# Optimization experiments

Hardware: AMD Instinct MI355X
Metric: run time of the kernel (lower is better)

Reference implementation:

```python
import jax, jax.numpy as jnp
import numpy as np

# config dims (see shape_source)
NO = 8        # Max_Object
NT = 32       # Max_Time
C = 512       # feat_dims
VD = 1024     # visual_dim
RD = 300      # self.nfeat (relation word-vector dim)
H = 4         # headnum
B = 8         # batch
No = NT * 2 * NO      # 512 object-graph nodes
Nr = NT * NO * NO     # 2048 relation-graph nodes


def _glorot(key, shape):
    fan_in = shape[0]
    return jax.random.normal(key, shape, dtype=jnp.float32) / np.sqrt(fan_in)


def setup_inputs() -> dict:
    key = jax.random.key(0)
    ks = jax.random.split(key, 18)
    inp = {
        "Ao": jax.random.uniform(ks[0], (B, No, No), dtype=jnp.float32),
        "srco": jax.random.normal(ks[1], (B, 1, 1, No, VD), dtype=jnp.float32),
        "Ar": jax.random.uniform(ks[2], (B, Nr, Nr), dtype=jnp.float32),
        "srcr": jax.random.normal(ks[3], (B, 1, 1, Nr, RD), dtype=jnp.float32),
        # GraphConvolution weights: gcl_o/gcl2_o and gcl_r/gcl2_r
        "Wo1": _glorot(ks[4], (VD, 1024)),
        "Wo2": _glorot(ks[5], (1024, C)),
        "Wr1": _glorot(ks[6], (RD, 1024)),
        "Wr2": _glorot(ks[7], (1024, C)),
        # MultiHeadAttention (e2n) projections
        "Wq": _glorot(ks[8], (C, C)), "bq": jnp.zeros((C,), jnp.float32),
        "Wk": _glorot(ks[9], (C, C)), "bk": jnp.zeros((C,), jnp.float32),
        "Wv": _glorot(ks[10], (C, C)), "bv": jnp.zeros((C,), jnp.float32),
        "Wp": _glorot(ks[11], (C, C)), "bp": jnp.zeros((C,), jnp.float32),
        # e2n_embed: Linear(2C -> C)
        "We": _glorot(ks[12], (2 * C, C)), "be": jnp.zeros((C,), jnp.float32),
    }
    return inp


def _gcn2(A, x, W1, W2):
    """Two stacked GraphConvolution layers with self-loops: relu((A+I) @ x @ W).
    A: (b,N,N), x: (b,N,Din). Vectorized over batch (torch code loops per-sample)."""
    eye = jnp.eye(A.shape[-1], dtype=A.dtype)
    Ah = A + eye
    h = jax.nn.relu(jnp.einsum('bij,bjd->bid', Ah, x @ W1))
    return jax.nn.relu(jnp.einsum('bij,bjd->bid', Ah, h @ W2))


def _mha(x, Wq, bq, Wk, bk, Wv, bv, Wp, bp):
    """Standard multi-head self-attention. x: (Bseg, S, C)."""
    Bs, S, _ = x.shape
    dh = C // H
    q = (x @ Wq + bq).reshape(Bs, S, H, dh)
    k = (x @ Wk + bk).reshape(Bs, S, H, dh)
    v = (x @ Wv + bv).reshape(Bs, S, H, dh)
    attn = jax.nn.softmax(jnp.einsum('bqhd,bkhd->bhqk', q, k) / np.sqrt(dh), axis=-1)
    o = jnp.einsum('bhqk,bkhd->bqhd', attn, v).reshape(Bs, S, C)
    return o @ Wp + bp


def _forward(Ao, srco, Ar, srcr, Wo1, Wo2, Wr1, Wr2,
             Wq, bq, Wk, bk, Wv, bv, Wp, bp, We, be):
    b = Ao.shape[0]
    # object-graph GCN (torch loops over batch; vectorized here)
    xo = srco[:, 0, 0, :, :VD]                       # (b, No, VD)
    srco_gcn = _gcn2(Ao, xo, Wo1, Wo2)               # (b, No, C)
    out_gcn_o = srco_gcn.reshape(b, NT, 2 * NO, C)
    # relation-graph GCN
    xr = srcr[:, 0, 0]                               # (b, Nr, RD)
    srcr_gcn = _gcn2(Ar, xr, Wr1, Wr2)               # (b, Nr, C)
    out_gcn_r = srcr_gcn.reshape(b, NT, NO * NO, C)
    # compute_e2n: segment-wise MHA over NO-token windows (torch loops over NO)
    r = out_gcn_r.reshape(b * NT, NO, NO, C)
    seg_a = r.reshape(b * NT * NO, NO, C)                      # rows of NOxNO grid
    a = _mha(seg_a, Wq, bq, Wk, bk, Wv, bv, Wp, bp).mean(axis=1)
    a = a.reshape(b * NT, NO, C)
    seg_o = jnp.swapaxes(r, 1, 2).reshape(b * NT * NO, NO, C)  # cols (permute 0,2,1,3)
    o = _mha(seg_o, Wq, bq, Wk, bk, Wv, bv, Wp, bp).mean(axis=1)
    o = o.reshape(b * NT, NO, C)
    tmp = jnp.concatenate([a, o], axis=1)                      # (b*NT, 2*NO, C)
    cat = jnp.concatenate([tmp, out_gcn_o.reshape(b * NT, 2 * NO, C)], axis=-1)
    out_e2n = cat @ We + be
    return out_e2n.reshape(b, NT, 2 * NO, C)


def reference(Ao, srco, Ar, srcr, Wo1, Wo2, Wr1, Wr2,
              Wq, bq, Wk, bk, Wv, bv, Wp, bp, We, be):
    return _forward(Ao, srco, Ar, srcr, Wo1, Wo2, Wr1, Wr2,
                    Wq, bq, Wk, bk, Wv, bv, Wp, bp, We, be)
```

## Files before the change

kernel.cpp:

```cpp
#include <hip/hip_runtime.h>
#include <hip/hip_bf16.h>


typedef __attribute__((ext_vector_type(4))) float f32x4;
typedef __attribute__((ext_vector_type(8))) short bf16x8s;

#define TILE 128
#define BKK 32
#define LDSS 40
#define LDSL 32

#if __has_builtin(__builtin_amdgcn_global_load_lds)
#define HAVE_GLL 1
#else
#define HAVE_GLL 0
#endif

__device__ inline void gll16(const __hip_bfloat16* g, __hip_bfloat16* l) {
#if HAVE_GLL
    __builtin_amdgcn_global_load_lds(
        (const __attribute__((address_space(1))) void*)g,
        (__attribute__((address_space(3))) void*)l,
        16, 0, 0);
#endif
}

__device__ inline void split2(float a, float b, unsigned& h, unsigned& l) {
    __hip_bfloat16 ha = __float2bfloat16(a), hb = __float2bfloat16(b);
    float ra = __bfloat162float(ha), rb = __bfloat162float(hb);
    __hip_bfloat16 la = __float2bfloat16(a - ra), lb = __float2bfloat16(b - rb);
    unsigned short uha = *(unsigned short*)&ha, uhb = *(unsigned short*)&hb;
    unsigned short ula = *(unsigned short*)&la, ulb = *(unsigned short*)&lb;
    h = (unsigned)uha | ((unsigned)uhb << 16);
    l = (unsigned)ula | ((unsigned)ulb << 16);
}

__device__ inline void splitw(float v, unsigned short& h, unsigned short& l) {
    __hip_bfloat16 hb = __float2bfloat16(v);
    __hip_bfloat16 lb = __float2bfloat16(v - __bfloat162float(hb));
    h = *(unsigned short*)&hb;
    l = *(unsigned short*)&lb;
}

__device__ inline void swz_block(int& bx, int& by, int& bz) {
    int gx = gridDim.x, gy = gridDim.y;
    int nwg = gx * gy * gridDim.z;
    int flat = bx + gx * (by + gy * bz);
    int cpx = nwg >> 3;
    int w = (flat & 7) * cpx + (flat >> 3);
    bx = w % gx;
    int t = w / gx;
    by = t % gy;
    bz = t / gy;
}

__global__ __launch_bounds__(256) void gemm_planes(
    const __hip_bfloat16* __restrict__ Aph, const __hip_bfloat16* __restrict__ Apl,
    long long sA, int lda,
    const __hip_bfloat16* __restrict__ BTh, const __hip_bfloat16* __restrict__ BTl,
    long long sBT, int ldbt,
    void* __restrict__ D, __hip_bfloat16* __restrict__ Dl_, long long sD, int ldd,
    const float* __restrict__ addN, long long sAddN, int ldaddN,
    const __hip_bfloat16* __restrict__ addTh, const __hip_bfloat16* __restrict__ addTl,
    long long sAddT, int ldaddT,
    const float* __restrict__ bias,
    int K, int relu, int outMode)
{
    __shared__ __hip_bfloat16 AhB[2][TILE * LDSL], AlB[2][TILE * LDSL];
    __shared__ __hip_bfloat16 BhB[2][TILE * LDSL], BlB[2][TILE * LDSL];

    int bx = blockIdx.x, by = blockIdx.y, bz = blockIdx.z;
    swz_block(bx, by, bz);

    const int tid  = threadIdx.x;
    const int lane = tid & 63;
    const int wave = tid >> 6;
    const int wm   = (wave >> 1) * 64;
    const int wn   = (wave & 1) * 64;
    const int row0 = by * TILE;
    const int col0 = bx * TILE;
    const int b    = bz;

    const __hip_bfloat16* Abh = Aph + (size_t)b * sA;
    const __hip_bfloat16* Abl = Apl + (size_t)b * sA;
    const __hip_bfloat16* Bbh = BTh + (size_t)b * sBT;
    const __hip_bfloat16* Bbl = BTl + (size_t)b * sBT;

    f32x4 acc[4][4];
#pragma unroll
    for (int i = 0; i < 4; ++i)
#pragma unroll
        for (int j = 0; j < 4; ++j) acc[i][j] = (f32x4){0.f, 0.f, 0.f, 0.f};

    const int quad = lane >> 4;
    const int l16  = lane & 15;

    const int m0  = wave * 16 + (lane >> 2);
    const int m1  = (wave + 4) * 16 + (lane >> 2);
    const int sl  = lane & 3;
    const int kq0 = sl ^ ((m0 >> 1) & 3);
    const int kq1 = sl ^ ((m1 >> 1) & 3);
    const size_t gA0 = (size_t)(row0 + m0) * lda + kq0 * 8;
    const size_t gA1 = (size_t)(row0 + m1) * lda + kq1 * 8;
    const size_t gB0 = (size_t)(col0 + m0) * ldbt + kq0 * 8;
    const size_t gB1 = (size_t)(col0 + m1) * ldbt + kq1 * 8;
    const int ldsc0 = wave * 512;
    const int ldsc1 = (wave + 4) * 512;

#if HAVE_GLL
#define STAGE(buf, kk) do { \
    gll16(Abh + gA0 + (kk), &AhB[buf][ldsc0]); \
    gll16(Abh + gA1 + (kk), &AhB[buf][ldsc1]); \
    gll16(Abl + gA0 + (kk), &AlB[buf][ldsc0]); \
    gll16(Abl + gA1 + (kk), &AlB[buf][ldsc1]); \
    gll16(Bbh + gB0 + (kk), &BhB[buf][ldsc0]); \
    gll16(Bbh + gB1 + (kk), &BhB[buf][ldsc1]); \
    gll16(Bbl + gB0 + (kk), &BlB[buf][ldsc0]); \
    gll16(Bbl + gB1 + (kk), &BlB[buf][ldsc1]); \
} while (0)
#define WAITVM8() asm volatile("s_waitcnt vmcnt(8)" ::: "memory")
#define WAITVM0() asm volatile("s_waitcnt vmcnt(0)" ::: "memory")
#else
#define STAGE(buf, kk) do { \
    *(uint4*)(&AhB[buf][m0 * LDSL + sl * 8]) = *(const uint4*)(Abh + gA0 + (kk)); \
    *(uint4*)(&AhB[buf][m1 * LDSL + sl * 8]) = *(const uint4*)(Abh + gA1 + (kk)); \
    *(uint4*)(&AlB[buf][m0 * LDSL + sl * 8]) = *(const uint4*)(Abl + gA0 + (kk)); \
    *(uint4*)(&AlB[buf][m1 * LDSL + sl * 8]) = *(const uint4*)(Abl + gA1 + (kk)); \
    *(uint4*)(&BhB[buf][m0 * LDSL + sl * 8]) = *(const uint4*)(Bbh + gB0 + (kk)); \
    *(uint4*)(&BhB[buf][m1 * LDSL + sl * 8]) = *(const uint4*)(Bbh + gB1 + (kk)); \
    *(uint4*)(&BlB[buf][m0 * LDSL + sl * 8]) = *(const uint4*)(Bbl + gB0 + (kk)); \
    *(uint4*)(&BlB[buf][m1 * LDSL + sl * 8]) = *(const uint4*)(Bbl + gB1 + (kk)); \
} while (0)
#define WAITVM8() asm volatile("" ::: "memory")
#define WAITVM0() asm volatile("" ::: "memory")
#endif

    const int nt = K / BKK;
    int cur = 0;

    STAGE(0, 0);
    STAGE(1, BKK);

    for (int t = 0; t < nt; ++t) {
        if (t + 1 < nt) { WAITVM8(); } else { WAITVM0(); }
        __builtin_amdgcn_s_barrier();

        const __hip_bfloat16* Ah = AhB[cur];
        const __hip_bfloat16* Al = AlB[cur];
        const __hip_bfloat16* Bh = BhB[cur];
        const __hip_bfloat16* Bl = BlB[cur];

        bf16x8s bhf[4], blf[4];
#pragma unroll
        for (int nt2 = 0; nt2 < 4; ++nt2) {
            int r = wn + nt2 * 16 + l16;
            int ss = (quad ^ ((r >> 1) & 3)) * 8;
            bhf[nt2] = *(const bf16x8s*)(&Bh[r * LDSL + ss]);
            blf[nt2] = *(const bf16x8s*)(&Bl[r * LDSL + ss]);
        }
#pragma unroll
        for (int mt = 0; mt < 4; ++mt) {
            int r = wm + mt * 16 + l16;
            int ss = (quad ^ ((r >> 1) & 3)) * 8;
            bf16x8s ahf = *(const bf16x8s*)(&Ah[r * LDSL + ss]);
            bf16x8s alf = *(const bf16x8s*)(&Al[r * LDSL + ss]);
#pragma unroll
            for (int nt2 = 0; nt2 < 4; ++nt2) {
                acc[mt][nt2] = __builtin_amdgcn_mfma_f32_16x16x32_bf16(ahf, bhf[nt2], acc[mt][nt2], 0, 0, 0);
                acc[mt][nt2] = __builtin_amdgcn_mfma_f32_16x16x32_bf16(ahf, blf[nt2], acc[mt][nt2], 0, 0, 0);
                acc[mt][nt2] = __builtin_amdgcn_mfma_f32_16x16x32_bf16(alf, bhf[nt2], acc[mt][nt2], 0, 0, 0);
            }
        }

        __builtin_amdgcn_s_barrier();
        if (t + 2 < nt) STAGE(cur, (t + 2) * BKK);
        cur ^= 1;
    }
#undef STAGE
#undef WAITVM8
#undef WAITVM0

    float* DbF = (float*)D + (size_t)b * sD;
    __hip_bfloat16* Dhb = (__hip_bfloat16*)D + (size_t)b * sD;
    __hip_bfloat16* Dlb = Dl_ ? Dl_ + (size_t)b * sD : nullptr;
    const float* AddN = addN ? addN + (size_t)b * sAddN : nullptr;
    const __hip_bfloat16* ATh = addTh ? addTh + (size_t)b * sAddT : nullptr;
    const __hip_bfloat16* ATl = addTl ? addTl + (size_t)b * sAddT : nullptr;
#pragma unroll
    for (int mt = 0; mt < 4; ++mt)
#pragma unroll
        for (int nt2 = 0; nt2 < 4; ++nt2)
#pragma unroll
            for (int r = 0; r < 4; ++r) {
                int m = row0 + wm + mt * 16 + quad * 4 + r;
                int n = col0 + wn + nt2 * 16 + l16;
                float v = acc[mt][nt2][r];
                if (AddN) v += AddN[(size_t)m * ldaddN + n];
                if (ATh) v += __bfloat162float(ATh[(size_t)n * ldaddT + m])
                            + __bfloat162float(ATl[(size_t)n * ldaddT + m]);
                if (bias) v += bias[n];
                if (relu && v < 0.f) v = 0.f;
                if (outMode == 0) {
                    DbF[(size_t)m * ldd + n] = v;
                } else {
                    unsigned short hh, ll;
                    splitw(v, hh, ll);
                    size_t o = (size_t)m * ldd + n;
                    *(unsigned short*)&Dhb[o] = hh;
                    *(unsigned short*)&Dlb[o] = ll;
                }
            }
}

__global__ __launch_bounds__(256) void gemm_bf16t(
    const __hip_bfloat16* __restrict__ A, int lda,
    const __hip_bfloat16* __restrict__ BT, int ldbt,
    void* __restrict__ D, int ldd,
    const float* __restrict__ bias,
    int K, int outF32)
{
    __shared__ __hip_bfloat16 AsB[2][TILE * LDSL];
    __shared__ __hip_bfloat16 BsB[2][TILE * LDSL];

    int bx = blockIdx.x, by = blockIdx.y, bz = blockIdx.z;
    swz_block(bx, by, bz);

    const int tid  = threadIdx.x;
    const int lane = tid & 63;
    const int wave = tid >> 6;
    const int wm   = (wave >> 1) * 64;
    const int wn   = (wave & 1) * 64;
    const int row0 = by * TILE;
    const int col0 = bx * TILE;

    f32x4 acc[4][4];
#pragma unroll
    for (int i = 0; i < 4; ++i)
#pragma unroll
        for (int j = 0; j < 4; ++j) acc[i][j] = (f32x4){0.f, 0.f, 0.f, 0.f};

    const int quad = lane >> 4;
    const int l16  = lane & 15;

    const int m0  = wave * 16 + (lane >> 2);
    const int m1  = (wave + 4) * 16 + (lane >> 2);
    const int sl  = lane & 3;
    const int kq0 = sl ^ ((m0 >> 1) & 3);
    const int kq1 = sl ^ ((m1 >> 1) & 3);
    const size_t gA0 = (size_t)(row0 + m0) * lda + kq0 * 8;
    const size_t gA1 = (size_t)(row0 + m1) * lda + kq1 * 8;
    const size_t gB0 = (size_t)(col0 + m0) * ldbt + kq0 * 8;
    const size_t gB1 = (size_t)(col0 + m1) * ldbt + kq1 * 8;
    const int ldsc0 = wave * 512;
    const int ldsc1 = (wave + 4) * 512;

#if HAVE_GLL
#define STAGE1(buf, kk) do { \
    gll16(A + gA0 + (kk), &AsB[buf][ldsc0]); \
    gll16(A + gA1 + (kk), &AsB[buf][ldsc1]); \
    gll16(BT + gB0 + (kk), &BsB[buf][ldsc0]); \
    gll16(BT + gB1 + (kk), &BsB[buf][ldsc1]); \
} while (0)
#define WAITVM4() asm volatile("s_waitcnt vmcnt(4)" ::: "memory")
#define WAITVM0() asm volatile("s_waitcnt vmcnt(0)" ::: "memory")
#else
#define STAGE1(buf, kk) do { \
    *(uint4*)(&AsB[buf][m0 * LDSL + sl * 8]) = *(const uint4*)(A + gA0 + (kk)); \
    *(uint4*)(&AsB[buf][m1 * LDSL + sl * 8]) = *(const uint4*)(A + gA1 + (kk)); \
    *(uint4*)(&BsB[buf][m0 * LDSL + sl * 8]) = *(const uint4*)(BT + gB0 + (kk)); \
    *(uint4*)(&BsB[buf][m1 * LDSL + sl * 8]) = *(const uint4*)(BT + gB1 + (kk)); \
} while (0)
#define WAITVM4() asm volatile("" ::: "memory")
#define WAITVM0() asm volatile("" ::: "memory")
#endif

    const int nt = K / BKK;
    int cur = 0;

    STAGE1(0, 0);
    STAGE1(1, BKK);

    for (int t = 0; t < nt; ++t) {
        if (t + 1 < nt) { WAITVM4(); } else { WAITVM0(); }
        __builtin_amdgcn_s_barrier();

        const __hip_bfloat16* As = AsB[cur];
        const __hip_bfloat16* Bs = BsB[cur];

        bf16x8s bfrag[4];
#pragma unroll
        for (int nt2 = 0; nt2 < 4; ++nt2) {
            int r = wn + nt2 * 16 + l16;
            int ss = (quad ^ ((r >> 1) & 3)) * 8;
            bfrag[nt2] = *(const bf16x8s*)(&Bs[r * LDSL + ss]);
        }
#pragma unroll
        for (int mt = 0; mt < 4; ++mt) {
            int r = wm + mt * 16 + l16;
            int ss = (quad ^ ((r >> 1) & 3)) * 8;
            bf16x8s afrag = *(const bf16x8s*)(&As[r * LDSL + ss]);
#pragma unroll
            for (int nt2 = 0; nt2 < 4; ++nt2)
                acc[mt][nt2] = __builtin_amdgcn_mfma_f32_16x16x32_bf16(
                    afrag, bfrag[nt2], acc[mt][nt2], 0, 0, 0);
        }

        __builtin_amdgcn_s_barrier();
        if (t + 2 < nt) STAGE1(cur, (t + 2) * BKK);
        cur ^= 1;
    }
#undef STAGE1
#undef WAITVM4
#undef WAITVM0

    float* DbF = (float*)D;
    __hip_bfloat16* Db16 = (__hip_bfloat16*)D;
#pragma unroll
    for (int mt = 0; mt < 4; ++mt)
#pragma unroll
        for (int nt2 = 0; nt2 < 4; ++nt2)
#pragma unroll
            for (int r = 0; r < 4; ++r) {
                int m = row0 + wm + mt * 16 + quad * 4 + r;
                int n = col0 + wn + nt2 * 16 + l16;
                float v = acc[mt][nt2][r];
                if (bias) v += bias[n];
                if (outF32) DbF[(size_t)m * ldd + n] = v;
                else        Db16[(size_t)m * ldd + n] = __float2bfloat16(v);
            }
}

__global__ __launch_bounds__(256) void gemm_asplit(
    const float* __restrict__ A, long long sA, int lda,
    const __hip_bfloat16* __restrict__ BTh, const __hip_bfloat16* __restrict__ BTl,
    long long sBT, int ldbt,
    __hip_bfloat16* __restrict__ Dh_, __hip_bfloat16* __restrict__ Dl_,
    long long sD, int ldd,
    const float* __restrict__ addN, long long sAddN, int ldaddN,
    const __hip_bfloat16* __restrict__ addTh, const __hip_bfloat16* __restrict__ addTl,
    long long sAddT, int ldaddT,
    int K, int relu)
{
    __shared__ __hip_bfloat16 Ah[TILE * LDSS], Al[TILE * LDSS];
    __shared__ __hip_bfloat16 Bh[TILE * LDSS], Bl[TILE * LDSS];

    const int tid  = threadIdx.x;
    const int lane = tid & 63;
    const int wave = tid >> 6;
    const int wm   = (wave >> 1) * 64;
    const int wn   = (wave & 1) * 64;
    const int row0 = blockIdx.y * TILE;
    const int col0 = blockIdx.x * TILE;
    const int b    = blockIdx.z;

    const float* Ab = A + (size_t)b * sA;
    const __hip_bfloat16* Bbh = BTh + (size_t)b * sBT;
    const __hip_bfloat16* Bbl = BTl + (size_t)b * sBT;

    f32x4 acc[4][4];
#pragma unroll
    for (int i = 0; i < 4; ++i)
#pragma unroll
        for (int j = 0; j < 4; ++j) acc[i][j] = (f32x4){0.f, 0.f, 0.f, 0.f};

    const int quad = lane >> 4;
    const int l16  = lane & 15;

    for (int k0 = 0; k0 < K; k0 += BKK) {
        __syncthreads();
#pragma unroll
        for (int it = 0; it < 2; ++it) {
            int task = tid + it * 256;
            int m = task >> 2, kq = task & 3;
            const float* ap = Ab + (size_t)(row0 + m) * lda + k0 + kq * 8;
            float4 v0 = *(const float4*)ap;
            float4 v1 = *(const float4*)(ap + 4);
            uint4 H, L;
            split2(v0.x, v0.y, H.x, L.x); split2(v0.z, v0.w, H.y, L.y);
            split2(v1.x, v1.y, H.z, L.z); split2(v1.z, v1.w, H.w, L.w);
            *(uint4*)(&Ah[m * LDSS + kq * 8]) = H;
            *(uint4*)(&Al[m * LDSS + kq * 8]) = L;
        }
#pragma unroll
        for (int it = 0; it < 2; ++it) {
            int task = tid + it * 256;
            int n = task >> 2, kq = task & 3;
            size_t off = (size_t)(col0 + n) * ldbt + k0 + kq * 8;
            *(uint4*)(&Bh[n * LDSS + kq * 8]) = *(const uint4*)(Bbh + off);
            *(uint4*)(&Bl[n * LDSS + kq * 8]) = *(const uint4*)(Bbl + off);
        }
        __syncthreads();

        bf16x8s ah[4], al[4], bh[4], bl[4];
#pragma unroll
        for (int mt = 0; mt < 4; ++mt) {
            int r = (wm + mt * 16 + l16) * LDSS + quad * 8;
            ah[mt] = *(const bf16x8s*)(&Ah[r]);
            al[mt] = *(const bf16x8s*)(&Al[r]);
        }
#pragma unroll
        for (int nt = 0; nt < 4; ++nt) {
            int r = (wn + nt * 16 + l16) * LDSS + quad * 8;
            bh[nt] = *(const bf16x8s*)(&Bh[r]);
            bl[nt] = *(const bf16x8s*)(&Bl[r]);
        }
#pragma unroll
        for (int mt = 0; mt < 4; ++mt)
#pragma unroll
            for (int nt = 0; nt < 4; ++nt) {
                acc[mt][nt] = __builtin_amdgcn_mfma_f32_16x16x32_bf16(ah[mt], bh[nt], acc[mt][nt], 0, 0, 0);
                acc[mt][nt] = __builtin_amdgcn_mfma_f32_16x16x32_bf16(ah[mt], bl[nt], acc[mt][nt], 0, 0, 0);
                acc[mt][nt] = __builtin_amdgcn_mfma_f32_16x16x32_bf16(al[mt], bh[nt], acc[mt][nt], 0, 0, 0);
            }
    }

    __hip_bfloat16* Dhb = Dh_ + (size_t)b * sD;
    __hip_bfloat16* Dlb = Dl_ + (size_t)b * sD;
    const float* AddN = addN ? addN + (size_t)b * sAddN : nullptr;
    const __hip_bfloat16* ATh = addTh ? addTh + (size_t)b * sAddT : nullptr;
    const __hip_bfloat16* ATl = addTl ? addTl + (size_t)b * sAddT : nullptr;
#pragma unroll
    for (int mt = 0; mt < 4; ++mt)
#pragma unroll
        for (int nt = 0; nt < 4; ++nt)
#pragma unroll
            for (int r = 0; r < 4; ++r) {
                int m = row0 + wm + mt * 16 + quad * 4 + r;
                int n = col0 + wn + nt * 16 + l16;
                float v = acc[mt][nt][r];
                if (AddN) v += AddN[(size_t)m * ldaddN + n];
                if (ATh) v += __bfloat162float(ATh[(size_t)n * ldaddT + m])
                            + __bfloat162float(ATl[(size_t)n * ldaddT + m]);
                if (relu && v < 0.f) v = 0.f;
                unsigned short hh, ll;
                splitw(v, hh, ll);
                size_t o = (size_t)m * ldd + n;
                *(unsigned short*)&Dhb[o] = hh;
                *(unsigned short*)&Dlb[o] = ll;
            }
}

__global__ __launch_bounds__(256) void padtrans_split(
    const float* __restrict__ src,
    __hip_bfloat16* __restrict__ dsth, __hip_bfloat16* __restrict__ dstl,
    int R, int C, int Rp, int Cp)
{
    __shared__ float T[64][65];
    const int t = threadIdx.x;
    const int tr = t >> 4, tc = t & 15;
    const int c0 = blockIdx.x * 64, r0 = blockIdx.y * 64;
    const size_t bat = blockIdx.z;
    const float* sb = src + bat * (size_t)R * C;
    __hip_bfloat16* dhb = dsth + bat * (size_t)Cp * Rp;
    __hip_bfloat16* dlb = dstl + bat * (size_t)Cp * Rp;

#pragma unroll
    for (int i = 0; i < 4; ++i) {
        int rr = tr + i * 16;
        int gr = r0 + rr;
        float v0 = 0.f, v1 = 0.f, v2 = 0.f, v3 = 0.f;
        if (gr < R) {
            int c = c0 + tc * 4;
            const float* s = sb + (size_t)gr * C + c;
            if (c + 0 < C) v0 = s[0];
            if (c + 1 < C) v1 = s[1];
            if (c + 2 < C) v2 = s[2];
            if (c + 3 < C) v3 = s[3];
        }
        T[rr][tc * 4 + 0] = v0; T[rr][tc * 4 + 1] = v1;
        T[rr][tc * 4 + 2] = v2; T[rr][tc * 4 + 3] = v3;
    }
    __syncthreads();
#pragma unroll
    for (int i = 0; i < 4; ++i) {
        int cc = tr + i * 16;
        float4 v = { T[tc * 4 + 0][cc], T[tc * 4 + 1][cc],
                     T[tc * 4 + 2][cc], T[tc * 4 + 3][cc] };
        ushort4 H, L;
        splitw(v.x, H.x, L.x); splitw(v.y, H.y, L.y);
        splitw(v.z, H.z, L.z); splitw(v.w, H.w, L.w);
        size_t off = (size_t)(c0 + cc) * Rp + r0 + tc * 4;
        *(ushort4*)(dhb + off) = H;
        *(ushort4*)(dlb + off) = L;
    }
}

__global__ __launch_bounds__(256) void padtrans_bf16(
    const float* __restrict__ src, __hip_bfloat16* __restrict__ dst,
    int R, int C, int Rp, int Cp)
{
    __shared__ float T[64][65];
    const int t = threadIdx.x;
    const int tr = t >> 4, tc = t & 15;
    const int c0 = blockIdx.x * 64, r0 = blockIdx.y * 64;

#pragma unroll
    for (int i = 0; i < 4; ++i) {
        int rr = tr + i * 16;
        int gr = r0 + rr;
        float v0 = 0.f, v1 = 0.f, v2 = 0.f, v3 = 0.f;
        if (gr < R) {
            int c = c0 + tc * 4;
            const float* s = src + (size_t)gr * C + c;
            if (c + 0 < C) v0 = s[0];
            if (c + 1 < C) v1 = s[1];
            if (c + 2 < C) v2 = s[2];
            if (c + 3 < C) v3 = s[3];
        }
        T[rr][tc * 4 + 0] = v0; T[rr][tc * 4 + 1] = v1;
        T[rr][tc * 4 + 2] = v2; T[rr][tc * 4 + 3] = v3;
    }
    __syncthreads();
#pragma unroll
    for (int i = 0; i < 4; ++i) {
        int cc = tr + i * 16;
        __hip_bfloat16 b0 = __float2bfloat16(T[tc * 4 + 0][cc]);
        __hip_bfloat16 b1 = __float2bfloat16(T[tc * 4 + 1][cc]);
        __hip_bfloat16 b2 = __float2bfloat16(T[tc * 4 + 2][cc]);
        __hip_bfloat16 b3 = __float2bfloat16(T[tc * 4 + 3][cc]);
        ushort4 o = { *(unsigned short*)&b0, *(unsigned short*)&b1,
                      *(unsigned short*)&b2, *(unsigned short*)&b3 };
        *(ushort4*)(dst + (size_t)(c0 + cc) * Rp + r0 + tc * 4) = o;
    }
}

__global__ __launch_bounds__(256) void gemm_bf16(
    const __hip_bfloat16* __restrict__ A, long long sA, int lda,
    const __hip_bfloat16* __restrict__ B, long long sB, int ldb,
    void* __restrict__ D, long long sD, int ldd,
    const __hip_bfloat16* __restrict__ addsrc, long long sAdd, int ldadd,
    const float* __restrict__ bias,
    int K, int relu, int outF32)
{
    __shared__ __hip_bfloat16 As[TILE * LDSS];
    __shared__ __hip_bfloat16 Bs[TILE * LDSS];

    int bx = blockIdx.x, by = blockIdx.y, bz = blockIdx.z;
    swz_block(bx, by, bz);

    const int tid  = threadIdx.x;
    const int lane = tid & 63;
    const int wave = tid >> 6;
    const int wm   = (wave >> 1) * 64;
    const int wn   = (wave & 1) * 64;
    const int row0 = by * TILE;
    const int col0 = bx * TILE;
    const int b    = bz;

    const __hip_bfloat16* Ab = A + (size_t)b * sA;
    const __hip_bfloat16* Bb = B + (size_t)b * sB;

    f32x4 acc[4][4];
#pragma unroll
    for (int i = 0; i < 4; ++i)
#pragma unroll
        for (int j = 0; j < 4; ++j) acc[i][j] = (f32x4){0.f, 0.f, 0.f, 0.f};

    const int quad = lane >> 4;
    const int l16  = lane & 15;

    for (int k0 = 0; k0 < K; k0 += BKK) {
        __syncthreads();
#pragma unroll
        for (int it = 0; it < 2; ++it) {
            int task = tid + it * 256;
            int m = task >> 2, kq = task & 3;
            uint4 val = *(const uint4*)(Ab + (size_t)(row0 + m) * lda + k0 + kq * 8);
            *(uint4*)(&As[m * LDSS + kq * 8]) = val;
        }
#pragma unroll
        for (int it = 0; it < 2; ++it) {
            int task = tid + it * 256;
            int kk = task >> 4, n8 = task & 15;
            uint4 val = *(const uint4*)(Bb + (size_t)(k0 + kk) * ldb + col0 + n8 * 8);
            const __hip_bfloat16* v16 = (const __hip_bfloat16*)&val;
#pragma unroll
            for (int u = 0; u < 8; ++u)
                Bs[(n8 * 8 + u) * LDSS + kk] = v16[u];
        }
        __syncthreads();

        bf16x8s afrag[4], bfrag[4];
#pragma unroll
        for (int mt = 0; mt < 4; ++mt)
            afrag[mt] = *(const bf16x8s*)(&As[(wm + mt * 16 + l16) * LDSS + quad * 8]);
#pragma unroll
        for (int nt = 0; nt < 4; ++nt)
            bfrag[nt] = *(const bf16x8s*)(&Bs[(wn + nt * 16 + l16) * LDSS + quad * 8]);
#pragma unroll
        for (int mt = 0; mt < 4; ++mt)
#pragma unroll
            for (int nt = 0; nt < 4; ++nt)
                acc[mt][nt] = __builtin_amdgcn_mfma_f32_16x16x32_bf16(
                    afrag[mt], bfrag[nt], acc[mt][nt], 0, 0, 0);
    }

    __hip_bfloat16* Db16 = (__hip_bfloat16*)D + (size_t)b * sD;
    float*          DbF  = (float*)D + (size_t)b * sD;
    const __hip_bfloat16* Addb = addsrc ? addsrc + (size_t)b * sAdd : nullptr;
#pragma unroll
    for (int mt = 0; mt < 4; ++mt)
#pragma unroll
        for (int nt = 0; nt < 4; ++nt)
#pragma unroll
            for (int r = 0; r < 4; ++r) {
                int m = row0 + wm + mt * 16 + quad * 4 + r;
                int n = col0 + wn + nt * 16 + l16;
                float v = acc[mt][nt][r];
                if (Addb) v += __bfloat162float(Addb[(size_t)m * ldadd + n]);
                if (bias) v += bias[n];
                if (relu && v < 0.f) v = 0.f;
                if (outF32) DbF[(size_t)m * ldd + n] = v;
                else        Db16[(size_t)m * ldd + n] = __float2bfloat16(v);
            }
}

__global__ void convert_kernel(const float* __restrict__ src,
                               __hip_bfloat16* __restrict__ dst, int n4)
{
    int i = blockIdx.x * blockDim.x + threadIdx.x;
    if (i >= n4) return;
    float4 v = ((const float4*)src)[i];
    __hip_bfloat16 t0 = __float2bfloat16(v.x), t1 = __float2bfloat16(v.y);
    __hip_bfloat16 t2 = __float2bfloat16(v.z), t3 = __float2bfloat16(v.w);
    ushort4 o = { *(unsigned short*)&t0, *(unsigned short*)&t1,
                  *(unsigned short*)&t2, *(unsigned short*)&t3 };
    ((ushort4*)dst)[i] = o;
}

__global__ void split_kernel(const float* __restrict__ src,
                             __hip_bfloat16* __restrict__ dh,
                             __hip_bfloat16* __restrict__ dl, int n4)
{
    int i = blockIdx.x * blockDim.x + threadIdx.x;
    if (i >= n4) return;
    float4 v = ((const float4*)src)[i];
    ushort4 H, L;
    splitw(v.x, H.x, L.x); splitw(v.y, H.y, L.y);
    splitw(v.z, H.z, L.z); splitw(v.w, H.w, L.w);
    ((ushort4*)dh)[i] = H;
    ((ushort4*)dl)[i] = L;
}

__global__ void bcat_kernel(const float* __restrict__ b0,
                            const float* __restrict__ b1,
                            const float* __restrict__ b2,
                            float* __restrict__ dst)
{
    int i = blockIdx.x * blockDim.x + threadIdx.x;
    if (i >= 1536) return;
    float v = (i < 512) ? b0[i] : (i < 1024) ? b1[i - 512] : b2[i - 1024];
    dst[i] = v;
}

__global__ __launch_bounds__(256) void attn_kernel(
    const float* __restrict__ q,
    const float* __restrict__ k,
    const float* __restrict__ v,
    int ld,
    __hip_bfloat16* __restrict__ abar)
{
    __shared__ float qs[8][512], ks[8][512], vs[8][512];
    __shared__ float sc[4][8][8];
    __shared__ float wb[4][8];

    const int tid  = threadIdx.x;
    const int mode = blockIdx.y;
    const int g    = blockIdx.x >> 3;
    const int idx  = blockIdx.x & 7;
    const int rowBase = g * 64;

    for (int t = tid; t < 512; t += 256) {
        int p = t >> 6, c8 = (t & 63) * 8;
        int row = (mode == 0) ? (rowBase + idx * 8 + p) : (rowBase + p * 8 + idx);
        const float* qp = q + (size_t)row * ld + c8;
        const float* kp = k + (size_t)row * ld + c8;
        const float* vp = v + (size_t)row * ld + c8;
        *(float4*)(&qs[p][c8])     = *(const float4*)(qp);
        *(float4*)(&qs[p][c8 + 4]) = *(const float4*)(qp + 4);
        *(float4*)(&ks[p][c8])     = *(const float4*)(kp);
        *(float4*)(&ks[p][c8 + 4]) = *(const float4*)(kp + 4);
        *(float4*)(&vs[p][c8])     = *(const float4*)(vp);
        *(float4*)(&vs[p][c8 + 4]) = *(const float4*)(vp + 4);
    }
    __syncthreads();

    {
        int h = tid >> 6, l = tid & 63;
        int i = l >> 3, j = l & 7;
        const float* qrow = &qs[i][h * 128];
        const float* krow = &ks[j][h * 128];
        float s = 0.f;
#pragma unroll
        for (int d = 0; d < 128; d += 4) {
            float4 qa = *(const float4*)(qrow + d);
            float4 kb = *(const float4*)(krow + d);
            s += qa.x * kb.x + qa.y * kb.y + qa.z * kb.z + qa.w * kb.w;
        }
        sc[h][i][j] = s * 0.08838834764831845f;
    }
    __syncthreads();

    if (tid < 32) {
        int h = tid >> 3, i = tid & 7;
        float mx = -1e30f;
#pragma unroll
        for (int j = 0; j < 8; ++j) mx = fmaxf(mx, sc[h][i][j]);
        float e[8], sum = 0.f;
#pragma unroll
        for (int j = 0; j < 8; ++j) { e[j] = __expf(sc[h][i][j] - mx); sum += e[j]; }
        float inv = 1.f / sum;
#pragma unroll
        for (int j = 0; j < 8; ++j) sc[h][i][j] = e[j] * inv;
    }
    __syncthreads();

    if (tid < 32) {
        int h = tid >> 3, j = tid & 7;
        float s = 0.f;
#pragma unroll
        for (int i = 0; i < 8; ++i) s += sc[h][i][j];
        wb[h][j] = s * 0.125f;
    }
    __syncthreads();

    {
        int orow = g * 16 + mode * 8 + idx;
        for (int c = tid; c < 512; c += 256) {
            int h = c >> 7;
            float o = 0.f;
#pragma unroll
            for (int j = 0; j < 8; ++j) o += wb[h][j] * vs[j][c];
            abar[(size_t)orow * 512 + c] = __float2bfloat16(o);
        }
    }
}


extern "C" void kernel_launch(void* const* d_in, const int* in_sizes, int n_in,
                              void* d_out, int out_size, void* d_ws, size_t ws_size,
                              hipStream_t stream)
{
    const float* Ao   = (const float*)d_in[0];
    const float* srco = (const float*)d_in[1];
    const float* Ar   = (const float*)d_in[2];
    const float* srcr = (const float*)d_in[3];
    const float* Wo1  = (const float*)d_in[4];
    const float* Wo2  = (const float*)d_in[5];
    const float* Wr1  = (const float*)d_in[6];
    const float* Wr2  = (const float*)d_in[7];
    const float* Wq   = (const float*)d_in[8];
    const float* bq   = (const float*)d_in[9];
    const float* Wk   = (const float*)d_in[10];
    const float* bk   = (const float*)d_in[11];
    const float* Wv   = (const float*)d_in[12];
    const float* bv   = (const float*)d_in[13];
    const float* Wp   = (const float*)d_in[14];
    const float* bp   = (const float*)d_in[15];
    const float* We   = (const float*)d_in[16];
    const float* be   = (const float*)d_in[17];
    float* out = (float*)d_out;

    char* ws = (char*)d_ws;
    const size_t R0 = 0;
    const size_t R1 = 67108864;
    const size_t R2 = 100663296;
    const size_t R3 = 134217728;
    const size_t R4 = 167772160;
    const size_t R5 = 192937984;
    const size_t R6 = 199491584;

    __hip_bfloat16* HRh = (__hip_bfloat16*)(ws + R0);
    __hip_bfloat16* HRl = HRh + 16777216;
    float* QKV  = (float*)(ws + R0);
    float* T2Rf = (float*)(ws + R1);
    __hip_bfloat16* Uh = (__hip_bfloat16*)(ws + R2);
    __hip_bfloat16* Ul = Uh + 6291456;
    __hip_bfloat16* T2RTh = (__hip_bfloat16*)(ws + R2);
    __hip_bfloat16* T2RTl = T2RTh + 8388608;
    float* bqkv = (float*)(ws + R2);
    __hip_bfloat16* GRh = (__hip_bfloat16*)(ws + R3);
    __hip_bfloat16* GRl = GRh + 8388608;
    __hip_bfloat16* XPTh = (__hip_bfloat16*)(ws + R4);
    __hip_bfloat16* XPTl = XPTh + 6291456;
    __hip_bfloat16* ABAR = (__hip_bfloat16*)(ws + R4);
    __hip_bfloat16* WPTh = (__hip_bfloat16*)(ws + R5);
    __hip_bfloat16* WPTl = WPTh + 327680;
    __hip_bfloat16* Wr2Th = (__hip_bfloat16*)(ws + R5 + 1310720);
    __hip_bfloat16* Wr2Tl = Wr2Th + 524288;
    __hip_bfloat16* WqkvTh = (__hip_bfloat16*)(ws + R5 + 3407872);
    __hip_bfloat16* WqkvTl = (__hip_bfloat16*)(ws + R5 + 4980736);
    __hip_bfloat16* Arh = (__hip_bfloat16*)(ws + R6);
    __hip_bfloat16* Arl = Arh + 33554432;
    const bool haveArPlanes = ws_size >= R6 + 2ull * 67108864ull;

    __hip_bfloat16* TO     = (__hip_bfloat16*)(ws + R2 + 0);
    __hip_bfloat16* HO     = (__hip_bfloat16*)(ws + R2 + 8388608);
    __hip_bfloat16* T2O    = (__hip_bfloat16*)(ws + R2 + 16777216);
    __hip_bfloat16* CAT    = (__hip_bfloat16*)(ws + R2 + 20971520);
    __hip_bfloat16* srcoB  = (__hip_bfloat16*)(ws + R2 + 29360128);
    __hip_bfloat16* AoB    = (__hip_bfloat16*)(ws + R2 + 37748736);
    __hip_bfloat16* Wo1BT  = (__hip_bfloat16*)(ws + R2 + 41943040);
    __hip_bfloat16* Wo2BT  = (__hip_bfloat16*)(ws + R2 + 44040192);
    __hip_bfloat16* WeBT   = (__hip_bfloat16*)(ws + R2 + 45088768);
    __hip_bfloat16* WpBT   = (__hip_bfloat16*)(ws + R2 + 46137344);

    dim3 blk(256);
    auto cvt = [&](const float* s, __hip_bfloat16* d, int n) {
        convert_kernel<<<dim3((n / 4 + 255) / 256), blk, 0, stream>>>(s, d, n / 4);
    };

    padtrans_split<<<dim3(6, 32, 8), blk, 0, stream>>>(srcr, XPTh, XPTl, 2048, 300, 2048, 384);
    padtrans_split<<<dim3(16, 5, 1), blk, 0, stream>>>(Wr1, WPTh, WPTl, 300, 1024, 320, 1024);
    padtrans_split<<<dim3(8, 16, 1), blk, 0, stream>>>(Wr2, Wr2Th, Wr2Tl, 1024, 512, 1024, 512);
    padtrans_split<<<dim3(8, 8, 1), blk, 0, stream>>>(Wq, WqkvTh, WqkvTl, 512, 512, 512, 512);
    padtrans_split<<<dim3(8, 8, 1), blk, 0, stream>>>(Wk, WqkvTh + 262144, WqkvTl + 262144, 512, 512, 512, 512);
    padtrans_split<<<dim3(8, 8, 1), blk, 0, stream>>>(Wv, WqkvTh + 524288, WqkvTl + 524288, 512, 512, 512, 512);

    if (haveArPlanes) {
        split_kernel<<<dim3(32768), blk, 0, stream>>>(Ar, Arh, Arl, 8388608);
        gemm_planes<<<dim3(3, 16, 8), blk, 0, stream>>>(
            Arh, Arl, 2048LL * 2048, 2048, XPTh, XPTl, 384LL * 2048, 2048,
            Uh, Ul, 2048LL * 384, 384,
            nullptr, 0, 0, XPTh, XPTl, 384LL * 2048, 2048,
            nullptr, 2048, 0, 1);
    } else {
        gemm_asplit<<<dim3(3, 16, 8), blk, 0, stream>>>(
            Ar, 2048LL * 2048, 2048, XPTh, XPTl, 384LL * 2048, 2048,
            Uh, Ul, 2048LL * 384, 384,
            nullptr, 0, 0, XPTh, XPTl, 384LL * 2048, 2048,
            2048, 0);
    }
    gemm_planes<<<dim3(8, 128, 1), blk, 0, stream>>>(
        Uh, Ul, 0, 384, WPTh, WPTl, 0, 320,
        HRh, HRl, 0, 1024,
        nullptr, 0, 0, nullptr, nullptr, 0, 0,
        nullptr, 320, 1, 1);
    gemm_planes<<<dim3(4, 128, 1), blk, 0, stream>>>(
        HRh, HRl, 0, 1024, Wr2Th, Wr2Tl, 0, 1024,
        T2Rf, nullptr, 0, 512,
        nullptr, 0, 0, nullptr, nullptr, 0, 0,
        nullptr, 1024, 0, 0);
    padtrans_split<<<dim3(8, 32, 8), blk, 0, stream>>>(T2Rf, T2RTh, T2RTl, 2048, 512, 2048, 512);
    if (haveArPlanes) {
        gemm_planes<<<dim3(4, 16, 8), blk, 0, stream>>>(
            Arh, Arl, 2048LL * 2048, 2048, T2RTh, T2RTl, 512LL * 2048, 2048,
            GRh, GRl, 2048LL * 512, 512,
            T2Rf, 2048LL * 512, 512, nullptr, nullptr, 0, 0,
            nullptr, 2048, 1, 1);
    } else {
        gemm_asplit<<<dim3(4, 16, 8), blk, 0, stream>>>(
            Ar, 2048LL * 2048, 2048, T2RTh, T2RTl, 512LL * 2048, 2048,
            GRh, GRl, 2048LL * 512, 512,
            T2Rf, 2048LL * 512, 512, nullptr, nullptr, 0, 0,
            2048, 1);
    }
    bcat_kernel<<<dim3(6), blk, 0, stream>>>(bq, bk, bv, bqkv);
    gemm_planes<<<dim3(12, 128, 1), blk, 0, stream>>>(
        GRh, GRl, 0, 512, WqkvTh, WqkvTl, 0, 512,
        QKV, nullptr, 0, 1536,
        nullptr, 0, 0, nullptr, nullptr, 0, 0,
        bqkv, 512, 0, 0);
    attn_kernel<<<dim3(2048, 2), blk, 0, stream>>>(QKV, QKV + 512, QKV + 1024, 1536, ABAR);

    cvt(srco, srcoB, 4194304);
    cvt(Ao, AoB, 2097152);
    padtrans_bf16<<<dim3(16, 16, 1), blk, 0, stream>>>(Wo1, Wo1BT, 1024, 1024, 1024, 1024);
    padtrans_bf16<<<dim3(8, 16, 1), blk, 0, stream>>>(Wo2, Wo2BT, 1024, 512, 1024, 512);
    padtrans_bf16<<<dim3(8, 16, 1), blk, 0, stream>>>(We, WeBT, 1024, 512, 1024, 512);
    padtrans_bf16<<<dim3(8, 8, 1), blk, 0, stream>>>(Wp, WpBT, 512, 512, 512, 512);
    gemm_bf16t<<<dim3(8, 32, 1), blk, 0, stream>>>(srcoB, 1024, Wo1BT, 1024,
        TO, 1024, nullptr, 1024, 0);
    gemm_bf16<<<dim3(8, 4, 8), blk, 0, stream>>>(AoB, 512LL * 512, 512, TO, 512LL * 1024, 1024,
        HO, 512LL * 1024, 1024, TO, 512LL * 1024, 1024, nullptr, 512, 1, 0);
    gemm_bf16t<<<dim3(4, 32, 1), blk, 0, stream>>>(HO, 1024, Wo2BT, 1024,
        T2O, 512, nullptr, 1024, 0);
    gemm_bf16<<<dim3(4, 4, 8), blk, 0, stream>>>(AoB, 512LL * 512, 512, T2O, 512LL * 512, 512,
        (void*)(CAT + 512), 512LL * 1024, 1024, T2O, 512LL * 512, 512, nullptr, 512, 1, 0);
    gemm_bf16t<<<dim3(4, 32, 1), blk, 0, stream>>>(ABAR, 512, WpBT, 512,
        CAT, 1024, bp, 512, 0);
    gemm_bf16t<<<dim3(4, 32, 1), blk, 0, stream>>>(CAT, 1024, WeBT, 1024,
        out, 512, be, 1024, 1);
}
```

Measured before the change: 1.015 ms.

## Split-K the Ar GEMM, batch two small GEMMs, use grid-stride conversion kernels

The first relation-graph GEMM (Ar × X, a 3x16x8 grid) is split along K into two halves, giving 768 blocks. Each half writes fp32 partials, and a new combine kernel sums them and splits the result into bf16 hi/lo planes. The Wo2 and Wp projections are merged into one gemm_bf16t launch selected by blockIdx.z. The convert and split kernels become grid-stride loops with a fixed 2048-block grid. Together these aim to fill the GPU better and cut launch count, at the cost of an extra fp32 partial buffer round trip and a changed summation order.

```diff
diff --git a/kernel.cpp b/kernel.cpp
--- a/kernel.cpp
+++ b/kernel.cpp
@@ -64,7 +64,8 @@
     const __hip_bfloat16* __restrict__ addTh, const __hip_bfloat16* __restrict__ addTl,
     long long sAddT, int ldaddT,
     const float* __restrict__ bias,
-    int K, int relu, int outMode)
+    int K, int relu, int outMode,
+    long long sKsplit, int splitk)
 {
     __shared__ __hip_bfloat16 AhB[2][TILE * LDSL], AlB[2][TILE * LDSL];
     __shared__ __hip_bfloat16 BhB[2][TILE * LDSL], BlB[2][TILE * LDSL];
@@ -79,7 +80,10 @@
     const int wn   = (wave & 1) * 64;
     const int row0 = by * TILE;
     const int col0 = bx * TILE;
-    const int b    = bz;
+
+    int b = bz, kz = 0, Keff = K;
+    if (splitk) { kz = bz & 1; b = bz >> 1; Keff = K >> 1; }
+    const int kbeg = kz * Keff;
 
     const __hip_bfloat16* Abh = Aph + (size_t)b * sA;
     const __hip_bfloat16* Abl = Apl + (size_t)b * sA;
@@ -135,11 +139,11 @@
 #define WAITVM0() asm volatile("" ::: "memory")
 #endif
 
-    const int nt = K / BKK;
+    const int nt = Keff / BKK;
     int cur = 0;
 
-    STAGE(0, 0);
-    STAGE(1, BKK);
+    STAGE(0, kbeg);
+    STAGE(1, kbeg + BKK);
 
     for (int t = 0; t < nt; ++t) {
         if (t + 1 < nt) { WAITVM8(); } else { WAITVM0(); }
@@ -173,19 +177,19 @@
         }
 
         __builtin_amdgcn_s_barrier();
-        if (t + 2 < nt) STAGE(cur, (t + 2) * BKK);
+        if (t + 2 < nt) STAGE(cur, kbeg + (t + 2) * BKK);
         cur ^= 1;
     }
 #undef STAGE
 #undef WAITVM8
 #undef WAITVM0
 
-    float* DbF = (float*)D + (size_t)b * sD;
+    float* DbF = (float*)D + (size_t)kz * sKsplit + (size_t)b * sD;
     __hip_bfloat16* Dhb = (__hip_bfloat16*)D + (size_t)b * sD;
     __hip_bfloat16* Dlb = Dl_ ? Dl_ + (size_t)b * sD : nullptr;
     const float* AddN = addN ? addN + (size_t)b * sAddN : nullptr;
-    const __hip_bfloat16* ATh = addTh ? addTh + (size_t)b * sAddT : nullptr;
-    const __hip_bfloat16* ATl = addTl ? addTl + (size_t)b * sAddT : nullptr;
+    const __hip_bfloat16* ATh = (addTh && kz == 0) ? addTh + (size_t)b * sAddT : nullptr;
+    const __hip_bfloat16* ATl = (addTl && kz == 0) ? addTl + (size_t)b * sAddT : nullptr;
 #pragma unroll
     for (int mt = 0; mt < 4; ++mt)
 #pragma unroll
@@ -213,17 +217,30 @@
 }
 
 __global__ __launch_bounds__(256) void gemm_bf16t(
-    const __hip_bfloat16* __restrict__ A, int lda,
-    const __hip_bfloat16* __restrict__ BT, int ldbt,
-    void* __restrict__ D, int ldd,
-    const float* __restrict__ bias,
-    int K, int outF32)
+    const __hip_bfloat16* __restrict__ A0, int lda0,
+    const __hip_bfloat16* __restrict__ BT0, int ldbt0,
+    void* __restrict__ D0, int ldd0,
+    const float* __restrict__ bias0, int K0, int outF32_0,
+    const __hip_bfloat16* __restrict__ A1, int lda1,
+    const __hip_bfloat16* __restrict__ BT1, int ldbt1,
+    void* __restrict__ D1, int ldd1,
+    const float* __restrict__ bias1, int K1, int outF32_1)
 {
     __shared__ __hip_bfloat16 AsB[2][TILE * LDSL];
     __shared__ __hip_bfloat16 BsB[2][TILE * LDSL];
 
     int bx = blockIdx.x, by = blockIdx.y, bz = blockIdx.z;
     swz_block(bx, by, bz);
+
+    const __hip_bfloat16* A  = (bz == 0) ? A0  : A1;
+    const __hip_bfloat16* BT = (bz == 0) ? BT0 : BT1;
+    void* D = (bz == 0) ? D0 : D1;
+    const float* bias = (bz == 0) ? bias0 : bias1;
+    const int lda  = (bz == 0) ? lda0  : lda1;
+    const int ldbt = (bz == 0) ? ldbt0 : ldbt1;
+    const int ldd  = (bz == 0) ? ldd0  : ldd1;
+    const int K    = (bz == 0) ? K0    : K1;
+    const int outF32 = (bz == 0) ? outF32_0 : outF32_1;
 
     const int tid  = threadIdx.x;
     const int lane = tid & 63;
@@ -618,28 +635,48 @@
 __global__ void convert_kernel(const float* __restrict__ src,
                                __hip_bfloat16* __restrict__ dst, int n4)
 {
-    int i = blockIdx.x * blockDim.x + threadIdx.x;
-    if (i >= n4) return;
-    float4 v = ((const float4*)src)[i];
-    __hip_bfloat16 t0 = __float2bfloat16(v.x), t1 = __float2bfloat16(v.y);
-    __hip_bfloat16 t2 = __float2bfloat16(v.z), t3 = __float2bfloat16(v.w);
-    ushort4 o = { *(unsigned short*)&t0, *(unsigned short*)&t1,
-                  *(unsigned short*)&t2, *(unsigned short*)&t3 };
-    ((ushort4*)dst)[i] = o;
+    for (int i = blockIdx.x * blockDim.x + threadIdx.x; i < n4;
+         i += gridDim.x * blockDim.x) {
+        float4 v = ((const float4*)src)[i];
+        __hip_bfloat16 t0 = __float2bfloat16(v.x), t1 = __float2bfloat16(v.y);
+        __hip_bfloat16 t2 = __float2bfloat16(v.z), t3 = __float2bfloat16(v.w);
+        ushort4 o = { *(unsigned short*)&t0, *(unsigned short*)&t1,
+                      *(unsigned short*)&t2, *(unsigned short*)&t3 };
+        ((ushort4*)dst)[i] = o;
+    }
 }
 
 __global__ void split_kernel(const float* __restrict__ src,
                              __hip_bfloat16* __restrict__ dh,
                              __hip_bfloat16* __restrict__ dl, int n4)
 {
-    int i = blockIdx.x * blockDim.x + threadIdx.x;
-    if (i >= n4) return;
-    float4 v = ((const float4*)src)[i];
-    ushort4 H, L;
-    splitw(v.x, H.x, L.x); splitw(v.y, H.y, L.y);
-    splitw(v.z, H.z, L.z); splitw(v.w, H.w, L.w);
-    ((ushort4*)dh)[i] = H;
-    ((ushort4*)dl)[i] = L;
+    for (int i = blockIdx.x * blockDim.x + threadIdx.x; i < n4;
+         i += gridDim.x * blockDim.x) {
+        float4 v = ((const float4*)src)[i];
+        ushort4 H, L;
+        splitw(v.x, H.x, L.x); splitw(v.y, H.y, L.y);
+        splitw(v.z, H.z, L.z); splitw(v.w, H.w, L.w);
+        ((ushort4*)dh)[i] = H;
+        ((ushort4*)dl)[i] = L;
+    }
+}
+
+__global__ void combine_split(const float* __restrict__ p0,
+                              const float* __restrict__ p1,
+                              __hip_bfloat16* __restrict__ dh,
+                              __hip_bfloat16* __restrict__ dl, int n4)
+{
+    for (int i = blockIdx.x * blockDim.x + threadIdx.x; i < n4;
+         i += gridDim.x * blockDim.x) {
+        float4 a = ((const float4*)p0)[i];
+        float4 b = ((const float4*)p1)[i];
+        float4 v = { a.x + b.x, a.y + b.y, a.z + b.z, a.w + b.w };
+        ushort4 H, L;
+        splitw(v.x, H.x, L.x); splitw(v.y, H.y, L.y);
+        splitw(v.z, H.z, L.z); splitw(v.w, H.w, L.w);
+        ((ushort4*)dh)[i] = H;
+        ((ushort4*)dl)[i] = L;
+    }
 }
 
 __global__ void bcat_kernel(const float* __restrict__ b0,
@@ -770,6 +807,7 @@
     const size_t R5 = 192937984;
     const size_t R6 = 199491584;
 
+    float* Pf = (float*)(ws + R0);
     __hip_bfloat16* HRh = (__hip_bfloat16*)(ws + R0);
     __hip_bfloat16* HRl = HRh + 16777216;
     float* QKV  = (float*)(ws + R0);
@@ -807,7 +845,7 @@
 
     dim3 blk(256);
     auto cvt = [&](const float* s, __hip_bfloat16* d, int n) {
-        convert_kernel<<<dim3((n / 4 + 255) / 256), blk, 0, stream>>>(s, d, n / 4);
+        convert_kernel<<<dim3(2048), blk, 0, stream>>>(s, d, n / 4);
     };
 
     padtrans_split<<<dim3(6, 32, 8), blk, 0, stream>>>(srcr, XPTh, XPTl, 2048, 300, 2048, 384);
@@ -818,12 +856,14 @@
     padtrans_split<<<dim3(8, 8, 1), blk, 0, stream>>>(Wv, WqkvTh + 524288, WqkvTl + 524288, 512, 512, 512, 512);
 
     if (haveArPlanes) {
-        split_kernel<<<dim3(32768), blk, 0, stream>>>(Ar, Arh, Arl, 8388608);
-        gemm_planes<<<dim3(3, 16, 8), blk, 0, stream>>>(
+        split_kernel<<<dim3(2048), blk, 0, stream>>>(Ar, Arh, Arl, 8388608);
+        gemm_planes<<<dim3(3, 16, 16), blk, 0, stream>>>(
             Arh, Arl, 2048LL * 2048, 2048, XPTh, XPTl, 384LL * 2048, 2048,
-            Uh, Ul, 2048LL * 384, 384,
+            Pf, nullptr, 2048LL * 384, 384,
             nullptr, 0, 0, XPTh, XPTl, 384LL * 2048, 2048,
-            nullptr, 2048, 0, 1);
+            nullptr, 2048, 0, 0, 6291456LL, 1);
+        combine_split<<<dim3(2048), blk, 0, stream>>>(
+            Pf, Pf + 6291456, Uh, Ul, 1572864);
     } else {
         gemm_asplit<<<dim3(3, 16, 8), blk, 0, stream>>>(
             Ar, 2048LL * 2048, 2048, XPTh, XPTl, 384LL * 2048, 2048,
@@ -835,19 +875,19 @@
         Uh, Ul, 0, 384, WPTh, WPTl, 0, 320,
         HRh, HRl, 0, 1024,
         nullptr, 0, 0, nullptr, nullptr, 0, 0,
-        nullptr, 320, 1, 1);
+        nullptr, 320, 1, 1, 0LL, 0);
     gemm_planes<<<dim3(4, 128, 1), blk, 0, stream>>>(
         HRh, HRl, 0, 1024, Wr2Th, Wr2Tl, 0, 1024,
         T2Rf, nullptr, 0, 512,
         nullptr, 0, 0, nullptr, nullptr, 0, 0,
-        nullptr, 1024, 0, 0);
+        nullptr, 1024, 0, 0, 0LL, 0);
     padtrans_split<<<dim3(8, 32, 8), blk, 0, stream>>>(T2Rf, T2RTh, T2RTl, 2048, 512, 2048, 512);
     if (haveArPlanes) {
         gemm_planes<<<dim3(4, 16, 8), blk, 0, stream>>>(
             Arh, Arl, 2048LL * 2048, 2048, T2RTh, T2RTl, 512LL * 2048, 2048,
             GRh, GRl, 2048LL * 512, 512,
             T2Rf, 2048LL * 512, 512, nullptr, nullptr, 0, 0,
-            nullptr, 2048, 1, 1);
+            nullptr, 2048, 1, 1, 0LL, 0);
     } else {
         gemm_asplit<<<dim3(4, 16, 8), blk, 0, stream>>>(
             Ar, 2048LL * 2048, 2048, T2RTh, T2RTl, 512LL * 2048, 2048,
@@ -860,7 +900,7 @@
         GRh, GRl, 0, 512, WqkvTh, WqkvTl, 0, 512,
         QKV, nullptr, 0, 1536,
         nullptr, 0, 0, nullptr, nullptr, 0, 0,
-        bqkv, 512, 0, 0);
+        bqkv, 512, 0, 0, 0LL, 0);
     attn_kernel<<<dim3(2048, 2), blk, 0, stream>>>(QKV, QKV + 512, QKV + 1024, 1536, ABAR);
 
     cvt(srco, srcoB, 4194304);
@@ -869,16 +909,17 @@
     padtrans_bf16<<<dim3(8, 16, 1), blk, 0, stream>>>(Wo2, Wo2BT, 1024, 512, 1024, 512);
     padtrans_bf16<<<dim3(8, 16, 1), blk, 0, stream>>>(We, WeBT, 1024, 512, 1024, 512);
     padtrans_bf16<<<dim3(8, 8, 1), blk, 0, stream>>>(Wp, WpBT, 512, 512, 512, 512);
-    gemm_bf16t<<<dim3(8, 32, 1), blk, 0, stream>>>(srcoB, 1024, Wo1BT, 1024,
-        TO, 1024, nullptr, 1024, 0);
+    gemm_bf16t<<<dim3(8, 32, 1), blk, 0, stream>>>(
+        srcoB, 1024, Wo1BT, 1024, TO, 1024, nullptr, 1024, 0,
+        nullptr, 0, nullptr, 0, nullptr, 0, nullptr, 0, 0);
     gemm_bf16<<<dim3(8, 4, 8), blk, 0, stream>>>(AoB, 512LL * 512, 512, TO, 512LL * 1024, 1024,
         HO, 512LL * 1024, 1024, TO, 512LL * 1024, 1024, nullptr, 512, 1, 0);
-    gemm_bf16t<<<dim3(4, 32, 1), blk, 0, stream>>>(HO, 1024, Wo2BT, 1024,
-        T2O, 512, nullptr, 1024, 0);
+    gemm_bf16t<<<dim3(4, 32, 2), blk, 0, stream>>>(
+        HO, 1024, Wo2BT, 1024, T2O, 512, nullptr, 1024, 0,
+        ABAR, 512, WpBT, 512, CAT, 1024, bp, 512, 0);
     gemm_bf16<<<dim3(4, 4, 8), blk, 0, stream>>>(AoB, 512LL * 512, 512, T2O, 512LL * 512, 512,
         (void*)(CAT + 512), 512LL * 1024, 1024, T2O, 512LL * 512, 512, nullptr, 512, 1, 0);
-    gemm_bf16t<<<dim3(4, 32, 1), blk, 0, stream>>>(ABAR, 512, WpBT, 512,
-        CAT, 1024, bp, 512, 0);
-    gemm_bf16t<<<dim3(4, 32, 1), blk, 0, stream>>>(CAT, 1024, WeBT, 1024,
-        out, 512, be, 1024, 1);
-}
+    gemm_bf16t<<<dim3(4, 32, 1), blk, 0, stream>>>(
+        CAT, 1024, WeBT, 1024, out, 512, be, 1024, 1,
+        nullptr, 0, nullptr, 0, nullptr, 0, nullptr, 0, 0);
+}
```

New measurement: 1.017 ms. No clear change (+0.2%).
